# Performance work log

Hardware: AMD Instinct MI355X
Metric: run time of the kernel (lower is better)

## Reference

```python
import jax, jax.numpy as jnp
import numpy as np

R = 7          # window size
HEADS = 8
HEAD_C = 32
SCALE = HEAD_C ** -0.5


def setup_inputs() -> dict:
    key = jax.random.key(0)
    k1, k2, k3, k4 = jax.random.split(key, 4)
    B, heads, H, C = 4, HEADS, 112, HEAD_C
    nW = (H // R) * (H // R)  # 256
    topk = 4
    q = jax.random.normal(k1, (B, heads, H, H, C), jnp.float32)
    k = jax.random.normal(k2, (B, heads, H, H, C), jnp.float32)
    v = jax.random.normal(k3, (B, heads, H, H, C), jnp.float32)
    indices = jax.random.randint(k4, (B, heads, nW, topk), 0, nW)
    return {"q": q, "k": k, "v": v, "indices": indices}


def reference(q, k, v, indices):
    r = R
    B, heads, H, W, C = q.shape
    nW = (H // r) * (W // r)
    w2 = r * r
    topk = indices.shape[-1]

    def partition(x):
        # (B, heads, H, W, C) -> (B, heads, nW, w2, C)
        x = x.reshape(B, heads, H // r, r, W // r, r, C)
        return x.transpose(0, 1, 2, 4, 3, 5, 6).reshape(B, heads, nW, w2, C)

    Q = partition(q)
    K = partition(k)
    V = partition(v)

    # Q -> (nW*B, heads, w2, C)
    Qw = Q.transpose(2, 0, 1, 3, 4).reshape(nW * B, heads, w2, C)

    # KV gather: for each (batch*head, window), gather topk other windows' KV
    idx = indices.reshape(B * heads, nW, topk)          # int indices into window dim
    n = B * heads

    def gather(kv):
        kvf = kv.reshape(n, nW, w2, C)
        # (n, nW, topk, w2, C): advanced indexing replicates torch.gather+expand
        g = kvf[jnp.arange(n)[:, None, None], idx]
        g = g.reshape(B, heads, nW, topk * w2, C)
        return g.transpose(2, 0, 1, 3, 4).reshape(nW * B, heads, topk * w2, C)

    Kg = gather(K)
    Vg = gather(V)

    # windowed softmax attention over gathered KV
    attn = jax.nn.softmax(jnp.einsum('bhqc,bhkc->bhqk', Qw, Kg) * SCALE, axis=-1)
    out = jnp.einsum('bhqk,bhkc->bhqc', attn, Vg)
    out = out.transpose(0, 2, 1, 3).reshape(nW * B, w2, heads * C)

    # combine windows back to (B, H, W, heads*C)
    out = out.reshape(nW, B, r, r, heads * C).transpose(1, 0, 2, 3, 4)
    out = out.reshape(B, H // r, W // r, r, r, heads * C)
    out = out.transpose(0, 1, 3, 2, 4, 5).reshape(B, H, W, heads * C)
    return out
```

## Files before the change

kernel.cpp:

```cpp
#include <hip/hip_runtime.h>
#include <hip/hip_bf16.h>

#define RR      7
#define NHEADS  8
#define CDIM    32
#define HDIM    112
#define NWIN    256
#define W2      49
#define TOPK    4
#define NKEY    196
#define NKROW   208
#define KLD     40
#define VLD     208
#define PLD     216
#define SCALE_F 0.17677669529663687f

typedef short  bf16x8  __attribute__((ext_vector_type(8)));
typedef float  f32x4   __attribute__((ext_vector_type(4)));
typedef unsigned short ushortv4 __attribute__((ext_vector_type(4)));

static __device__ __forceinline__ unsigned short f2bf(float f) {
    unsigned u = __builtin_bit_cast(unsigned, f);
    u += 0x7FFFu + ((u >> 16) & 1u);
    return (unsigned short)(u >> 16);
}

__global__ __launch_bounds__(256, 4)
void wsa_kernel(const float* __restrict__ qg, const float* __restrict__ kg,
                const float* __restrict__ vg, const int* __restrict__ ind,
                float* __restrict__ outg)
{
    __shared__ __align__(16) unsigned char LDSBUF[40960];
    unsigned short* Vts = (unsigned short*)LDSBUF;
    unsigned short* Ks  = (unsigned short*)(LDSBUF + 13312);
    unsigned short* Ps  = (unsigned short*)(LDSBUF + 13312);

    int bid  = blockIdx.x;
    int nbid = (bid & 7) * 1024 + (bid >> 3);
    int w  = nbid & 255;
    int bh = nbid >> 8;
    int h  = bh & 7;
    int b  = bh >> 3;
    int wy = w >> 4, wx = w & 15;

    const int t = threadIdx.x;
    const int wave = t >> 6, lane = t & 63;
    const int l15 = lane & 15, lg = lane >> 4;
    const size_t slice = (size_t)HDIM * HDIM * CDIM;
    const float* qb = qg + (size_t)bh * slice;
    const float* kb = kg + (size_t)bh * slice;
    const float* vb = vg + (size_t)bh * slice;
    const int*  idx = ind + ((size_t)bh * NWIN + w) * TOPK;

    int qrow = wave * 16 + l15; if (qrow > 48) qrow = 48;
    int qi = qrow / RR, qj = qrow - qi * RR;
    const float* qp = qb + ((size_t)((wy * RR + qi) * HDIM + wx * RR + qj)) * CDIM + lg * 8;
    float4 qlo = *(const float4*)qp;
    float4 qhi = *(const float4*)(qp + 4);
    bf16x8 afrag = { (short)f2bf(qlo.x * SCALE_F), (short)f2bf(qlo.y * SCALE_F),
                     (short)f2bf(qlo.z * SCALE_F), (short)f2bf(qlo.w * SCALE_F),
                     (short)f2bf(qhi.x * SCALE_F), (short)f2bf(qhi.y * SCALE_F),
                     (short)f2bf(qhi.z * SCALE_F), (short)f2bf(qhi.w * SCALE_F) };

    int4 w4 = *(const int4*)idx;
#pragma unroll
    for (int it = 0; it < 7; ++it) {
        int task = t + it * 256;
        bool live = (task < NKROW * 8);
        int key = task >> 3, c4 = (task & 7) << 2;
        bool pad = (key >= NKEY) || !live;
        int kk = pad ? 0 : key;
        int tw = kk / W2;
        int m  = kk - tw * W2;
        int widx = (tw == 0) ? w4.x : (tw == 1) ? w4.y : (tw == 2) ? w4.z : w4.w;
        int i = m / RR, j = m - i * RR;
        size_t off = ((size_t)(((widx >> 4) * RR + i) * HDIM + (widx & 15) * RR + j)) * CDIM + c4;
        float4 kv = {0.f, 0.f, 0.f, 0.f}, vv = {0.f, 0.f, 0.f, 0.f};
        if (!pad) { kv = *(const float4*)(kb + off); vv = *(const float4*)(vb + off); }
        if (live) {
            ushortv4 ko = { f2bf(kv.x), f2bf(kv.y), f2bf(kv.z), f2bf(kv.w) };
            *(ushortv4*)&Ks[key * KLD + c4] = ko;
            Vts[(c4 + 0) * VLD + key] = f2bf(vv.x);
            Vts[(c4 + 1) * VLD + key] = f2bf(vv.y);
            Vts[(c4 + 2) * VLD + key] = f2bf(vv.z);
            Vts[(c4 + 3) * VLD + key] = f2bf(vv.w);
        }
    }
    __syncthreads();

    f32x4 zero4 = {0.f, 0.f, 0.f, 0.f};
    f32x4 acc[13];
#pragma unroll
    for (int nt = 0; nt < 13; ++nt) acc[nt] = zero4;
#pragma unroll
    for (int nt = 0; nt < 13; ++nt) {
        bf16x8 bfrag = *(const bf16x8*)&Ks[(nt * 16 + l15) * KLD + lg * 8];
        acc[nt] = __builtin_amdgcn_mfma_f32_16x16x32_bf16(afrag, bfrag, acc[nt], 0, 0, 0);
    }

    float inv[4];
    const bool tail_ok = (l15 < 4);
#pragma unroll
    for (int r = 0; r < 4; ++r) {
        float mx = -1e30f;
#pragma unroll
        for (int nt = 0; nt < 12; ++nt) mx = fmaxf(mx, acc[nt][r]);
        if (tail_ok) mx = fmaxf(mx, acc[12][r]);
#pragma unroll
        for (int off = 1; off < 16; off <<= 1) mx = fmaxf(mx, __shfl_xor(mx, off));
        float s = 0.f;
#pragma unroll
        for (int nt = 0; nt < 13; ++nt) {
            float p = (nt < 12 || tail_ok) ? __expf(acc[nt][r] - mx) : 0.f;
            acc[nt][r] = p;
            s += p;
        }
#pragma unroll
        for (int off = 1; off < 16; off <<= 1) s += __shfl_xor(s, off);
        inv[r] = 1.f / s;
    }

    __syncthreads();

#pragma unroll
    for (int r = 0; r < 4; ++r) {
        int rowm = wave * 16 + lg * 4 + r;
#pragma unroll
        for (int nt = 0; nt < 13; ++nt)
            Ps[rowm * PLD + nt * 16 + l15] = f2bf(acc[nt][r]);
    }
    __syncthreads();

    f32x4 oacc[2] = {zero4, zero4};
#pragma unroll
    for (int kt = 0; kt < 6; ++kt) {
        bf16x8 pa = *(const bf16x8*)&Ps[(wave * 16 + l15) * PLD + kt * 32 + lg * 8];
#pragma unroll
        for (int n2 = 0; n2 < 2; ++n2) {
            bf16x8 vbf = *(const bf16x8*)&Vts[(n2 * 16 + l15) * VLD + kt * 32 + lg * 8];
            oacc[n2] = __builtin_amdgcn_mfma_f32_16x16x32_bf16(pa, vbf, oacc[n2], 0, 0, 0);
        }
    }
    {
        bf16x8 z8 = {0, 0, 0, 0, 0, 0, 0, 0};
        bf16x8 pa = z8, vb0 = z8, vb1 = z8;
        if (lg < 2) {
            pa  = *(const bf16x8*)&Ps[(wave * 16 + l15) * PLD + 192 + lg * 8];
            vb0 = *(const bf16x8*)&Vts[l15 * VLD + 192 + lg * 8];
            vb1 = *(const bf16x8*)&Vts[(16 + l15) * VLD + 192 + lg * 8];
        }
        oacc[0] = __builtin_amdgcn_mfma_f32_16x16x32_bf16(pa, vb0, oacc[0], 0, 0, 0);
        oacc[1] = __builtin_amdgcn_mfma_f32_16x16x32_bf16(pa, vb1, oacc[1], 0, 0, 0);
    }

#pragma unroll
    for (int r = 0; r < 4; ++r) {
        int rowm = wave * 16 + lg * 4 + r;
        if (rowm < W2) {
            int i = rowm / RR, j = rowm - i * RR;
            int y = wy * RR + i, x = wx * RR + j;
            float* op = outg + (((size_t)b * HDIM + y) * HDIM + x) * (NHEADS * CDIM) + h * CDIM;
            op[l15]      = oacc[0][r] * inv[r];
            op[16 + l15] = oacc[1][r] * inv[r];
        }
    }
}

extern "C" void kernel_launch(void* const* d_in, const int* in_sizes, int n_in,
                              void* d_out, int out_size, void* d_ws, size_t ws_size,
                              hipStream_t stream) {
    const float* q   = (const float*)d_in[0];
    const float* k   = (const float*)d_in[1];
    const float* v   = (const float*)d_in[2];
    const int*   idx = (const int*)d_in[3];
    float* out = (float*)d_out;
    wsa_kernel<<<dim3(8192), dim3(256), 0, stream>>>(q, k, v, idx, out);
}
```

Measured before the change: 224.7 us.

## Transpose QK MFMA, swizzle LDS layouts, and pack bf16 conversions

Swaps the MFMA operands so each lane holds scores for one query column, which cuts the softmax reductions to two cross-group shuffles and lets probabilities be written as packed 8-byte stores. K, V^T and P tiles now use XOR-swizzled LDS rows in place of padded strides, and each thread loads eight contiguous floats. V is transposed in registers (four keys per thread) before packed stores. The hardware v_cvt_pk_bf16_f32 instruction replaces the manual rounding, and the last wave overlaps rows 33-48 so no row is clamped. The aim is fewer LDS bank conflicts, fewer instructions and fewer shuffles, at the cost of more register pressure and more complex indexing.

Result: faster. 214.1 us (-4.8%).

```diff
diff --git a/kernel.cpp b/kernel.cpp
--- a/kernel.cpp
+++ b/kernel.cpp
@@ -1,5 +1,4 @@
 #include <hip/hip_runtime.h>
-#include <hip/hip_bf16.h>
 
 #define RR      7
 #define NHEADS  8
@@ -9,31 +8,32 @@
 #define W2      49
 #define TOPK    4
 #define NKEY    196
-#define NKROW   208
-#define KLD     40
-#define VLD     208
-#define PLD     216
 #define SCALE_F 0.17677669529663687f
 
-typedef short  bf16x8  __attribute__((ext_vector_type(8)));
-typedef float  f32x4   __attribute__((ext_vector_type(4)));
-typedef unsigned short ushortv4 __attribute__((ext_vector_type(4)));
-
-static __device__ __forceinline__ unsigned short f2bf(float f) {
-    unsigned u = __builtin_bit_cast(unsigned, f);
-    u += 0x7FFFu + ((u >> 16) & 1u);
-    return (unsigned short)(u >> 16);
+#define VT_BASE 0
+#define K_BASE  14336
+#define P_BASE  14336
+#define LDS_SZ  36288
+
+typedef short    bf16x8 __attribute__((ext_vector_type(8)));
+typedef float    f32x4  __attribute__((ext_vector_type(4)));
+typedef unsigned u32x2  __attribute__((ext_vector_type(2)));
+typedef unsigned u32x4  __attribute__((ext_vector_type(4)));
+
+static __device__ __forceinline__ unsigned cvt_pk(float lo, float hi) {
+    unsigned r;
+    asm("v_cvt_pk_bf16_f32 %0, %1, %2" : "=v"(r) : "v"(lo), "v"(hi));
+    return r;
 }
+
+#define SWZ448(row, inner) ((row)*448 + ((inner) ^ (((row)&3) << 4)))
 
 __global__ __launch_bounds__(256, 4)
 void wsa_kernel(const float* __restrict__ qg, const float* __restrict__ kg,
                 const float* __restrict__ vg, const int* __restrict__ ind,
                 float* __restrict__ outg)
 {
-    __shared__ __align__(16) unsigned char LDSBUF[40960];
-    unsigned short* Vts = (unsigned short*)LDSBUF;
-    unsigned short* Ks  = (unsigned short*)(LDSBUF + 13312);
-    unsigned short* Ps  = (unsigned short*)(LDSBUF + 13312);
+    __shared__ __align__(16) unsigned char lds[LDS_SZ];
 
     int bid  = blockIdx.x;
     int nbid = (bid & 7) * 1024 + (bid >> 3);
@@ -52,40 +52,73 @@
     const float* vb = vg + (size_t)bh * slice;
     const int*  idx = ind + ((size_t)bh * NWIN + w) * TOPK;
 
-    int qrow = wave * 16 + l15; if (qrow > 48) qrow = 48;
-    int qi = qrow / RR, qj = qrow - qi * RR;
-    const float* qp = qb + ((size_t)((wy * RR + qi) * HDIM + wx * RR + qj)) * CDIM + lg * 8;
-    float4 qlo = *(const float4*)qp;
-    float4 qhi = *(const float4*)(qp + 4);
-    bf16x8 afrag = { (short)f2bf(qlo.x * SCALE_F), (short)f2bf(qlo.y * SCALE_F),
-                     (short)f2bf(qlo.z * SCALE_F), (short)f2bf(qlo.w * SCALE_F),
-                     (short)f2bf(qhi.x * SCALE_F), (short)f2bf(qhi.y * SCALE_F),
-                     (short)f2bf(qhi.z * SCALE_F), (short)f2bf(qhi.w * SCALE_F) };
-
     int4 w4 = *(const int4*)idx;
-#pragma unroll
-    for (int it = 0; it < 7; ++it) {
+    const float4 z4 = {0.f, 0.f, 0.f, 0.f};
+
+    const int qbase = (wave < 3) ? wave * 16 : 33;
+    bf16x8 bq;
+    {
+        int qrow = qbase + l15;
+        int qi = qrow / RR, qj = qrow - qi * RR;
+        const float* qp = qb + (size_t)((wy * RR + qi) * HDIM + wx * RR + qj) * CDIM + lg * 8;
+        float4 qa = ((const float4*)qp)[0];
+        float4 qc = ((const float4*)qp)[1];
+        union { u32x4 u; bf16x8 v; } qu;
+        qu.u = (u32x4){ cvt_pk(qa.x * SCALE_F, qa.y * SCALE_F),
+                        cvt_pk(qa.z * SCALE_F, qa.w * SCALE_F),
+                        cvt_pk(qc.x * SCALE_F, qc.y * SCALE_F),
+                        cvt_pk(qc.z * SCALE_F, qc.w * SCALE_F) };
+        bq = qu.v;
+    }
+
+#pragma unroll
+    for (int it = 0; it < 4; ++it) {
         int task = t + it * 256;
-        bool live = (task < NKROW * 8);
-        int key = task >> 3, c4 = (task & 7) << 2;
-        bool pad = (key >= NKEY) || !live;
-        int kk = pad ? 0 : key;
-        int tw = kk / W2;
-        int m  = kk - tw * W2;
-        int widx = (tw == 0) ? w4.x : (tw == 1) ? w4.y : (tw == 2) ? w4.z : w4.w;
-        int i = m / RR, j = m - i * RR;
-        size_t off = ((size_t)(((widx >> 4) * RR + i) * HDIM + (widx & 15) * RR + j)) * CDIM + c4;
-        float4 kv = {0.f, 0.f, 0.f, 0.f}, vv = {0.f, 0.f, 0.f, 0.f};
-        if (!pad) { kv = *(const float4*)(kb + off); vv = *(const float4*)(vb + off); }
-        if (live) {
-            ushortv4 ko = { f2bf(kv.x), f2bf(kv.y), f2bf(kv.z), f2bf(kv.w) };
-            *(ushortv4*)&Ks[key * KLD + c4] = ko;
-            Vts[(c4 + 0) * VLD + key] = f2bf(vv.x);
-            Vts[(c4 + 1) * VLD + key] = f2bf(vv.y);
-            Vts[(c4 + 2) * VLD + key] = f2bf(vv.z);
-            Vts[(c4 + 3) * VLD + key] = f2bf(vv.w);
-        }
-    }
+        if (task < 832) {
+            int key = task >> 2, c8 = task & 3;
+            float4 a = z4, c = z4;
+            if (key < NKEY) {
+                int tw = key / W2, m = key - tw * W2;
+                int widx = (tw == 0) ? w4.x : (tw == 1) ? w4.y : (tw == 2) ? w4.z : w4.w;
+                int i = m / RR, j = m - i * RR;
+                const float* p = kb + (size_t)(((widx >> 4) * RR + i) * HDIM +
+                                              (widx & 15) * RR + j) * CDIM + c8 * 8;
+                a = ((const float4*)p)[0];
+                c = ((const float4*)p)[1];
+            }
+            u32x4 pk = { cvt_pk(a.x, a.y), cvt_pk(a.z, a.w),
+                         cvt_pk(c.x, c.y), cvt_pk(c.z, c.w) };
+            *(u32x4*)(lds + K_BASE + key * 64 + ((c8 * 16) ^ ((key & 3) << 4))) = pk;
+        }
+    }
+
+    if (t < 224) {
+        int kgp = t >> 2, c8 = t & 3;
+        float va[4][8];
+#pragma unroll
+        for (int s = 0; s < 4; ++s) {
+            int key = kgp * 4 + s;
+            float4 lo = z4, hi = z4;
+            if (key < NKEY) {
+                int tw = key / W2, m = key - tw * W2;
+                int widx = (tw == 0) ? w4.x : (tw == 1) ? w4.y : (tw == 2) ? w4.z : w4.w;
+                int i = m / RR, j = m - i * RR;
+                const float* p = vb + (size_t)(((widx >> 4) * RR + i) * HDIM +
+                                              (widx & 15) * RR + j) * CDIM + c8 * 8;
+                lo = ((const float4*)p)[0];
+                hi = ((const float4*)p)[1];
+            }
+            *(float4*)&va[s][0] = lo;
+            *(float4*)&va[s][4] = hi;
+        }
+#pragma unroll
+        for (int j = 0; j < 8; ++j) {
+            int c = c8 * 8 + j;
+            u32x2 pk = { cvt_pk(va[0][j], va[1][j]), cvt_pk(va[2][j], va[3][j]) };
+            *(u32x2*)(lds + VT_BASE + SWZ448(c, kgp * 8)) = pk;
+        }
+    }
+
     __syncthreads();
 
     f32x4 zero4 = {0.f, 0.f, 0.f, 0.f};
@@ -94,74 +127,83 @@
     for (int nt = 0; nt < 13; ++nt) acc[nt] = zero4;
 #pragma unroll
     for (int nt = 0; nt < 13; ++nt) {
-        bf16x8 bfrag = *(const bf16x8*)&Ks[(nt * 16 + l15) * KLD + lg * 8];
-        acc[nt] = __builtin_amdgcn_mfma_f32_16x16x32_bf16(afrag, bfrag, acc[nt], 0, 0, 0);
-    }
-
-    float inv[4];
-    const bool tail_ok = (l15 < 4);
-#pragma unroll
-    for (int r = 0; r < 4; ++r) {
-        float mx = -1e30f;
-#pragma unroll
-        for (int nt = 0; nt < 12; ++nt) mx = fmaxf(mx, acc[nt][r]);
-        if (tail_ok) mx = fmaxf(mx, acc[12][r]);
-#pragma unroll
-        for (int off = 1; off < 16; off <<= 1) mx = fmaxf(mx, __shfl_xor(mx, off));
-        float s = 0.f;
-#pragma unroll
-        for (int nt = 0; nt < 13; ++nt) {
-            float p = (nt < 12 || tail_ok) ? __expf(acc[nt][r] - mx) : 0.f;
+        bf16x8 ka = *(const bf16x8*)(lds + K_BASE + (nt * 16 + l15) * 64 +
+                                     ((lg * 16) ^ ((l15 & 3) << 4)));
+        acc[nt] = __builtin_amdgcn_mfma_f32_16x16x32_bf16(ka, bq, acc[nt], 0, 0, 0);
+    }
+
+    float mx = -1e30f;
+#pragma unroll
+    for (int nt = 0; nt < 12; ++nt)
+#pragma unroll
+        for (int r = 0; r < 4; ++r) mx = fmaxf(mx, acc[nt][r]);
+    if (lg == 0) {
+#pragma unroll
+        for (int r = 0; r < 4; ++r) mx = fmaxf(mx, acc[12][r]);
+    }
+    mx = fmaxf(mx, __shfl_xor(mx, 16));
+    mx = fmaxf(mx, __shfl_xor(mx, 32));
+
+    float s = 0.f;
+#pragma unroll
+    for (int nt = 0; nt < 12; ++nt)
+#pragma unroll
+        for (int r = 0; r < 4; ++r) {
+            float p = __expf(acc[nt][r] - mx);
             acc[nt][r] = p;
             s += p;
         }
 #pragma unroll
-        for (int off = 1; off < 16; off <<= 1) s += __shfl_xor(s, off);
-        inv[r] = 1.f / s;
-    }
+    for (int r = 0; r < 4; ++r) {
+        float p = (lg == 0) ? __expf(acc[12][r] - mx) : 0.f;
+        acc[12][r] = p;
+        s += p;
+    }
+    s += __shfl_xor(s, 16);
+    s += __shfl_xor(s, 32);
+    const float invs = 1.0f / s;
 
     __syncthreads();
 
+    const int q = qbase + l15;
+    unsigned char* prow = lds + P_BASE + q * 448;
+    const int qx = (q & 3) << 4;
+    const int lgs = lg * 8;
+#pragma unroll
+    for (int nt = 0; nt < 13; ++nt) {
+        u32x2 pk = { cvt_pk(acc[nt][0] * invs, acc[nt][1] * invs),
+                     cvt_pk(acc[nt][2] * invs, acc[nt][3] * invs) };
+        *(u32x2*)(prow + ((nt * 32 + lgs) ^ qx)) = pk;
+    }
+    {
+        u32x2 zz = {0u, 0u};
+        *(u32x2*)(prow + ((13 * 32 + lgs) ^ qx)) = zz;
+    }
+    __syncthreads();
+
+    f32x4 o0 = zero4, o1 = zero4;
+    const int vx = (l15 & 3) << 4;
+#pragma unroll
+    for (int kt = 0; kt < 7; ++kt) {
+        bf16x8 pa = *(const bf16x8*)(prow + ((kt * 64 + 16 * lg) ^ qx));
+        bf16x8 v0 = *(const bf16x8*)(lds + VT_BASE + l15 * 448 +
+                                     ((kt * 64 + 16 * lg) ^ vx));
+        bf16x8 v1 = *(const bf16x8*)(lds + VT_BASE + (16 + l15) * 448 +
+                                     ((kt * 64 + 16 * lg) ^ vx));
+        o0 = __builtin_amdgcn_mfma_f32_16x16x32_bf16(pa, v0, o0, 0, 0, 0);
+        o1 = __builtin_amdgcn_mfma_f32_16x16x32_bf16(pa, v1, o1, 0, 0, 0);
+    }
+
 #pragma unroll
     for (int r = 0; r < 4; ++r) {
-        int rowm = wave * 16 + lg * 4 + r;
-#pragma unroll
-        for (int nt = 0; nt < 13; ++nt)
-            Ps[rowm * PLD + nt * 16 + l15] = f2bf(acc[nt][r]);
-    }
-    __syncthreads();
-
-    f32x4 oacc[2] = {zero4, zero4};
-#pragma unroll
-    for (int kt = 0; kt < 6; ++kt) {
-        bf16x8 pa = *(const bf16x8*)&Ps[(wave * 16 + l15) * PLD + kt * 32 + lg * 8];
-#pragma unroll
-        for (int n2 = 0; n2 < 2; ++n2) {
-            bf16x8 vbf = *(const bf16x8*)&Vts[(n2 * 16 + l15) * VLD + kt * 32 + lg * 8];
-            oacc[n2] = __builtin_amdgcn_mfma_f32_16x16x32_bf16(pa, vbf, oacc[n2], 0, 0, 0);
-        }
-    }
-    {
-        bf16x8 z8 = {0, 0, 0, 0, 0, 0, 0, 0};
-        bf16x8 pa = z8, vb0 = z8, vb1 = z8;
-        if (lg < 2) {
-            pa  = *(const bf16x8*)&Ps[(wave * 16 + l15) * PLD + 192 + lg * 8];
-            vb0 = *(const bf16x8*)&Vts[l15 * VLD + 192 + lg * 8];
-            vb1 = *(const bf16x8*)&Vts[(16 + l15) * VLD + 192 + lg * 8];
-        }
-        oacc[0] = __builtin_amdgcn_mfma_f32_16x16x32_bf16(pa, vb0, oacc[0], 0, 0, 0);
-        oacc[1] = __builtin_amdgcn_mfma_f32_16x16x32_bf16(pa, vb1, oacc[1], 0, 0, 0);
-    }
-
-#pragma unroll
-    for (int r = 0; r < 4; ++r) {
-        int rowm = wave * 16 + lg * 4 + r;
-        if (rowm < W2) {
+        int rowm = qbase + lg * 4 + r;
+        bool doit = (wave < 3) || (lg == 3 && r == 3);
+        if (doit) {
             int i = rowm / RR, j = rowm - i * RR;
-            int y = wy * RR + i, x = wx * RR + j;
-            float* op = outg + (((size_t)b * HDIM + y) * HDIM + x) * (NHEADS * CDIM) + h * CDIM;
-            op[l15]      = oacc[0][r] * inv[r];
-            op[16 + l15] = oacc[1][r] * inv[r];
+            float* op = outg + (((size_t)b * HDIM + wy * RR + i) * HDIM + wx * RR + j)
+                              * (NHEADS * CDIM) + h * CDIM;
+            op[l15]      = o0[r];
+            op[16 + l15] = o1[r];
         }
     }
 }
```
